# Kernel optimization log

Measured on AMD Instinct MI355X. Metric: run time of the kernel, lower is better.

The kernel has to match this reference:

```python
import jax, jax.numpy as jnp
import numpy as np

B, H, L, P = 16, 256, 8192, 64  # batch, d_input, seq_len, d_state


def setup_inputs() -> dict:
    key = jax.random.key(0)
    k1, k2, k3, k4, k5, k6 = jax.random.split(key, 6)
    u = jax.random.normal(k1, (B, H, L), dtype=jnp.float32)
    # diagonal SSM poles on an annulus inside the unit disk (stable discrete dynamics)
    radius = jax.random.uniform(k2, (P,), minval=0.5, maxval=0.99)
    theta = jax.random.uniform(k3, (P,), minval=0.0, maxval=2.0 * np.pi)
    A_re = (radius * jnp.cos(theta)).astype(jnp.float32)
    A_im = (radius * jnp.sin(theta)).astype(jnp.float32)
    # combined input/output mixing W = C*B, complex (H, P)
    BC_re = (jax.random.normal(k4, (H, P)) / np.sqrt(P)).astype(jnp.float32)
    BC_im = (jax.random.normal(k5, (H, P)) / np.sqrt(P)).astype(jnp.float32)
    # D skip vector: uniform_ring(min_radius=0.0, max_radius=1.0, field='real')
    D = jax.random.uniform(k6, (H,), minval=0.0, maxval=1.0, dtype=jnp.float32)
    return {"u": u, "A_re": A_re, "A_im": A_im, "BC_re": BC_re, "BC_im": BC_im, "D": D}


def reference(u, A_re, A_im, BC_re, BC_im, D):
    # Vandermonde kernel: k[h, l] = sum_p BC[h, p] * A[p]**l, computed stably via exp(l*log A)
    A = jax.lax.complex(A_re, A_im)                      # (P,)
    logA = jnp.log(A)                                    # (P,) complex
    ell = jnp.arange(L, dtype=jnp.float32)               # (L,)
    V = jnp.exp(logA[:, None] * ell[None, :])            # (P, L) complex Vandermonde
    BC = jax.lax.complex(BC_re, BC_im)                   # (H, P)
    k = jnp.einsum('hp,pl->hl', BC, V)                   # (H, L) complex kernel
    # circular FFT convolution (same-length fft/ifft as the torch code)
    u_s = jnp.fft.fft(u, axis=-1)                        # (B, H, L) complex
    k_s = jnp.fft.fft(k, axis=-1)                        # (H, L) complex
    y = jnp.fft.ifft(u_s * k_s[None, :, :], axis=-1).real
    y = y + D[None, :, None] * u                         # D*u skip
    return jnp.tanh(y)                                   # activation (dropout=0 -> identity)
```

## Files before the change

### kernel.cpp

```cpp
#include <hip/hip_runtime.h>
#include <cmath>


typedef _Float16 half8 __attribute__((ext_vector_type(8)));
typedef _Float16 half4v __attribute__((ext_vector_type(4)));
typedef _Float16 half2v __attribute__((ext_vector_type(2)));
typedef float floatx16 __attribute__((ext_vector_type(16)));

#define NC 64
#define CM 128
#define A2_BYTES ((size_t)256 * 128 * 256 * 2)
#define W_BYTES  ((size_t)128 * 128 * 2)
#define AM_OFF   (A2_BYTES + W_BYTES)

#define SWH(r, c) ((((r) << 7)) | ((c) ^ (((r) & 15) << 3)))

__device__ __forceinline__ float fast_tanh(float x) {
    float e2 = __expf(2.0f * x);
    return 1.0f - 2.0f / (e2 + 1.0f);
}

__global__ void fftconv_prep(const float* __restrict__ A_re, const float* __restrict__ A_im,
                             const float* __restrict__ BC_re, const float* __restrict__ BC_im,
                             const float* __restrict__ Dv, char* __restrict__ ws) {
    __shared__ float rr[64], th[64], br[64], bi[64];
    __shared__ float kk[CM];
    const int h = blockIdx.x, tid = threadIdx.x;
    if (tid < 64) {
        float x = A_re[tid], y = A_im[tid];
        rr[tid] = log2f(sqrtf(x * x + y * y));
        th[tid] = atan2f(y, x);
        br[tid] = BC_re[h * 64 + tid];
        bi[tid] = BC_im[h * 64 + tid];
    }
    __syncthreads();
    if (tid < CM) {
        float d = (float)tid, s = 0.f;
        for (int p = 0; p < 64; ++p) {
            float mag = exp2f(d * rr[p]);
            float ang = d * th[p];
            s += mag * (br[p] * cosf(ang) - bi[p] * sinf(ang));
        }
        kk[tid] = s;
    }
    __syncthreads();
    _Float16* A2 = (_Float16*)ws + (size_t)h * 128 * 256;
    const float Dh = Dv[h];
    for (int idx = tid; idx < 128 * 128; idx += 256) {
        int r = idx >> 7, pc = idx & 127, p = pc & 63;
        float e = (float)(r + 1);
        float mag = exp2f(e * rr[p]);
        float ang = e * th[p];
        float cr = mag * cosf(ang), ci = mag * sinf(ang);
        float val = (pc < 64) ? (br[p] * cr - bi[p] * ci) : -(br[p] * ci + bi[p] * cr);
        int cn = ((pc & 63) << 1) | (pc >> 6);
        A2[r * 256 + cn] = (_Float16)val;
    }
    for (int idx = tid; idx < 128 * 128; idx += 256) {
        int r = idx >> 7, j = idx & 127;
        float v = (j <= r) ? kk[r - j] : 0.f;
        if (j == r) v += Dh;
        A2[r * 256 + CM + j] = (_Float16)v;
    }
    if (h == 0) {
        _Float16* W = (_Float16*)(ws + A2_BYTES);
        for (int idx = tid; idx < 128 * 128; idx += 256) {
            int pc = idx >> 7, j = idx & 127, p = pc & 63;
            float e = (float)(127 - j);
            float mag = exp2f(e * rr[p]);
            float ang = e * th[p];
            float v = (pc < 64) ? mag * cosf(ang) : mag * sinf(ang);
            int rn = ((pc & 63) << 1) | (pc >> 6);
            W[rn * 128 + j] = (_Float16)v;
        }
        if (tid < 64) {
            float mag = exp2f(128.f * rr[tid]);
            float ang = 128.f * th[tid];
            float* aM = (float*)(ws + AM_OFF);
            aM[tid] = mag * cosf(ang);
            aM[64 + tid] = mag * sinf(ang);
        }
    }
}

__global__ __launch_bounds__(256, 3)
void fftconv_main(const float* __restrict__ u, const char* __restrict__ ws,
                  float* __restrict__ out) {
    __shared__ __align__(16) _Float16 u16[2][NC * CM];
    __shared__ __align__(16) _Float16 S16[NC * CM];

    const int tid = threadIdx.x;
    const int lane = tid & 63;
    const int wv = tid >> 6;
    const int h = blockIdx.x & 255;
    const int bbg = blockIdx.x >> 8;

    const int mrow = (wv << 5) + (lane & 31);
    const int kh = (lane >> 5) << 3;
    const int ncol = lane & 31;

    const _Float16* Wg = (const _Float16*)(ws + A2_BYTES) + (size_t)mrow * CM + kh;
    const _Float16* Ag = (const _Float16*)ws + ((size_t)h * CM + mrow) * 256 + kh;

    const float* ub0 = u + ((size_t)((bbg * 2 + 0) * 256) + h) * 8192;
    const float* ub1 = u + ((size_t)((bbg * 2 + 1) * 256) + h) * 8192;

    float4 uvA[8];
#pragma unroll
    for (int i = 0; i < 8; ++i) uvA[i] = ((const float4*)ub0)[i * 256 + tid];
    half8 wf[8], tf[8];
#pragma unroll
    for (int s = 0; s < 8; ++s) wf[s] = *(const half8*)(Wg + (s << 4));
#pragma unroll
    for (int s = 0; s < 8; ++s) tf[s] = *(const half8*)(Ag + CM + (s << 4));

#pragma unroll
    for (int i = 0; i < 8; ++i) {
        int e4 = i * 256 + tid;
        int c = e4 >> 5, j = (e4 << 2) & 127;
        half4v hv = { (_Float16)uvA[i].x, (_Float16)uvA[i].y,
                      (_Float16)uvA[i].z, (_Float16)uvA[i].w };
        *(half4v*)&u16[0][SWH(c, j)] = hv;
    }
    float4 uvB[8];
#pragma unroll
    for (int i = 0; i < 8; ++i) uvB[i] = ((const float4*)ub1)[i * 256 + tid];
    half8 gf[8];
    __syncthreads();

#pragma unroll
    for (int sq = 0; sq < 2; ++sq) {
        const _Float16* ub16 = u16[sq];

        {
            floatx16 a0 = {}; floatx16 a1 = {};
#pragma unroll
            for (int s = 0; s < 8; ++s) {
                int k0 = (s << 4) + kh;
                half8 b0 = *(const half8*)&ub16[SWH(ncol, k0)];
                half8 b1 = *(const half8*)&ub16[SWH(ncol + 32, k0)];
                a0 = __builtin_amdgcn_mfma_f32_32x32x16_f16(wf[s], b0, a0, 0, 0, 0);
                a1 = __builtin_amdgcn_mfma_f32_32x32x16_f16(wf[s], b1, a1, 0, 0, 0);
            }
            const int pc0 = (wv << 5) + ((lane >> 5) << 2);
#pragma unroll
            for (int g = 0; g < 4; ++g) {
                half4v h0 = { (_Float16)a0[4 * g + 0], (_Float16)a0[4 * g + 1],
                              (_Float16)a0[4 * g + 2], (_Float16)a0[4 * g + 3] };
                *(half4v*)&S16[SWH(ncol, pc0 + 8 * g)] = h0;
                half4v h1 = { (_Float16)a1[4 * g + 0], (_Float16)a1[4 * g + 1],
                              (_Float16)a1[4 * g + 2], (_Float16)a1[4 * g + 3] };
                *(half4v*)&S16[SWH(ncol + 32, pc0 + 8 * g)] = h1;
            }
        }
        if (sq == 0) {
#pragma unroll
            for (int i = 0; i < 8; ++i) {
                int e4 = i * 256 + tid;
                int c = e4 >> 5, j = (e4 << 2) & 127;
                half4v hv = { (_Float16)uvB[i].x, (_Float16)uvB[i].y,
                              (_Float16)uvB[i].z, (_Float16)uvB[i].w };
                *(half4v*)&u16[1][SWH(c, j)] = hv;
            }
        }
        __syncthreads();

        float er[16], ei[16];
        {
            const float* aM = (const float*)(ws + AM_OFF);
            const float amr = aM[lane], ami = aM[64 + lane];
            const int cbase = wv << 4;
            float sr = 0.f, si = 0.f, pr = 1.f, pi = 0.f;
#pragma unroll
            for (int d = 0; d < 8; ++d) {
                int cc = (cbase - 1 - d) & 63;
                half2v xv = *(const half2v*)&S16[SWH(cc, lane << 1)];
                float xr = (float)xv.x, xi = (float)xv.y;
                sr = fmaf(pr, xr, fmaf(-pi, xi, sr));
                si = fmaf(pr, xi, fmaf(pi, xr, si));
                float npr = pr * amr - pi * ami;
                float npi = pr * ami + pi * amr;
                pr = npr; pi = npi;
            }
            er[0] = sr; ei[0] = si;
#pragma unroll
            for (int i = 1; i < 16; ++i) {
                half2v xv = *(const half2v*)&S16[SWH(cbase + i - 1, lane << 1)];
                float xr = (float)xv.x, xi = (float)xv.y;
                er[i] = fmaf(amr, er[i - 1], fmaf(-ami, ei[i - 1], xr));
                ei[i] = fmaf(amr, ei[i - 1], fmaf(ami, er[i - 1], xi));
            }
        }
        __syncthreads();

        if (sq == 0) {
#pragma unroll
            for (int s = 0; s < 8; ++s) gf[s] = *(const half8*)(Ag + (s << 4));
        }

#pragma unroll
        for (int i = 0; i < 16; ++i) {
            int c = (wv << 4) + i;
            half2v ev = { (_Float16)er[i], (_Float16)ei[i] };
            *(half2v*)&S16[SWH(c, lane << 1)] = ev;
        }
        __syncthreads();

        {
            floatx16 y0 = {}; floatx16 y1 = {};
#pragma unroll
            for (int s = 0; s < 8; ++s) {
                int k0 = (s << 4) + kh;
                half8 b0 = *(const half8*)&S16[SWH(ncol, k0)];
                half8 b1 = *(const half8*)&S16[SWH(ncol + 32, k0)];
                y0 = __builtin_amdgcn_mfma_f32_32x32x16_f16(gf[s], b0, y0, 0, 0, 0);
                y1 = __builtin_amdgcn_mfma_f32_32x32x16_f16(gf[s], b1, y1, 0, 0, 0);
            }
#pragma unroll
            for (int s = 0; s < 8; ++s) {
                int k0 = (s << 4) + kh;
                half8 b0 = *(const half8*)&ub16[SWH(ncol, k0)];
                half8 b1 = *(const half8*)&ub16[SWH(ncol + 32, k0)];
                y0 = __builtin_amdgcn_mfma_f32_32x32x16_f16(tf[s], b0, y0, 0, 0, 0);
                y1 = __builtin_amdgcn_mfma_f32_32x32x16_f16(tf[s], b1, y1, 0, 0, 0);
            }
            float* yb = out + ((size_t)((bbg * 2 + sq) * 256) + h) * 8192;
            const int r0 = (wv << 5) + ((lane >> 5) << 2);
#pragma unroll
            for (int g = 0; g < 4; ++g) {
                float4 o0;
                o0.x = fast_tanh(y0[4 * g + 0]); o0.y = fast_tanh(y0[4 * g + 1]);
                o0.z = fast_tanh(y0[4 * g + 2]); o0.w = fast_tanh(y0[4 * g + 3]);
                *(float4*)(yb + (size_t)ncol * CM + r0 + 8 * g) = o0;
                float4 o1;
                o1.x = fast_tanh(y1[4 * g + 0]); o1.y = fast_tanh(y1[4 * g + 1]);
                o1.z = fast_tanh(y1[4 * g + 2]); o1.w = fast_tanh(y1[4 * g + 3]);
                *(float4*)(yb + (size_t)(ncol + 32) * CM + r0 + 8 * g) = o1;
            }
        }
        if (sq == 0) __syncthreads();
    }
}

extern "C" void kernel_launch(void* const* d_in, const int* in_sizes, int n_in,
                              void* d_out, int out_size, void* d_ws, size_t ws_size,
                              hipStream_t stream) {
    const float* u     = (const float*)d_in[0];
    const float* A_re  = (const float*)d_in[1];
    const float* A_im  = (const float*)d_in[2];
    const float* BC_re = (const float*)d_in[3];
    const float* BC_im = (const float*)d_in[4];
    const float* Dv    = (const float*)d_in[5];
    float* out = (float*)d_out;
    char* ws = (char*)d_ws;

    hipLaunchKernelGGL(fftconv_prep, dim3(256), dim3(256), 0, stream,
                       A_re, A_im, BC_re, BC_im, Dv, ws);
    hipLaunchKernelGGL(fftconv_main, dim3(2048), dim3(256), 0, stream,
                       u, ws, out);
}
```

Baseline: 350.9 us.

## Stream four sequences per block with async global-to-LDS DMA prefetch

Each block now handles four batch sequences instead of two, so the grid is halved and the per-(h) W/A fragments are loaded once and reused across more sequences. Input rows are fetched with global_load_lds directly into a swizzled fp32 LDS tile. The fetch for the next sequence is issued mid-iteration so it overlaps the scan and the second GEMM. The chunk scan is fused into one streaming loop without er/ei register arrays, and barriers use explicit lgkmcnt waits. This trades occupancy (launch bounds 3 to 2, larger LDS) and half the grid parallelism for fewer redundant loads and overlapped memory traffic.

Result: no change. 355.1 us (+1.2%).

```diff
diff --git a/kernel.cpp b/kernel.cpp
--- a/kernel.cpp
+++ b/kernel.cpp
@@ -9,15 +9,29 @@
 
 #define NC 64
 #define CM 128
+#define NSEQ 4
 #define A2_BYTES ((size_t)256 * 128 * 256 * 2)
 #define W_BYTES  ((size_t)128 * 128 * 2)
 #define AM_OFF   (A2_BYTES + W_BYTES)
 
 #define SWH(r, c) ((((r) << 7)) | ((c) ^ (((r) & 15) << 3)))
+#define SWF(c, q4) (((c) << 7) | ((((q4) ^ ((c) & 31))) << 2))
+
+#define BAR_LGKM() do { \
+    asm volatile("s_waitcnt lgkmcnt(0)" ::: "memory"); \
+    __builtin_amdgcn_sched_barrier(0); \
+    __builtin_amdgcn_s_barrier(); \
+} while (0)
 
 __device__ __forceinline__ float fast_tanh(float x) {
     float e2 = __expf(2.0f * x);
     return 1.0f - 2.0f / (e2 + 1.0f);
+}
+
+__device__ __forceinline__ void dma16(const void* g, void* l) {
+    __builtin_amdgcn_global_load_lds(
+        (const __attribute__((address_space(1))) void*)g,
+        (__attribute__((address_space(3))) void*)l, 16, 0, 0);
 }
 
 __global__ void fftconv_prep(const float* __restrict__ A_re, const float* __restrict__ A_im,
@@ -83,10 +97,11 @@
     }
 }
 
-__global__ __launch_bounds__(256, 3)
+__global__ __launch_bounds__(256, 2)
 void fftconv_main(const float* __restrict__ u, const char* __restrict__ ws,
                   float* __restrict__ out) {
-    __shared__ __align__(16) _Float16 u16[2][NC * CM];
+    __shared__ __align__(16) float    u32t[NC * CM];
+    __shared__ __align__(16) _Float16 u16t[NC * CM];
     __shared__ __align__(16) _Float16 S16[NC * CM];
 
     const int tid = threadIdx.x;
@@ -101,44 +116,48 @@
 
     const _Float16* Wg = (const _Float16*)(ws + A2_BYTES) + (size_t)mrow * CM + kh;
     const _Float16* Ag = (const _Float16*)ws + ((size_t)h * CM + mrow) * 256 + kh;
-
-    const float* ub0 = u + ((size_t)((bbg * 2 + 0) * 256) + h) * 8192;
-    const float* ub1 = u + ((size_t)((bbg * 2 + 1) * 256) + h) * 8192;
-
-    float4 uvA[8];
-#pragma unroll
-    for (int i = 0; i < 8; ++i) uvA[i] = ((const float4*)ub0)[i * 256 + tid];
-    half8 wf[8], tf[8];
+    const float* aM = (const float*)(ws + AM_OFF);
+    const float amr = aM[lane], ami = aM[64 + lane];
+
+    half8 wf[8], tf[8], gf[8];
 #pragma unroll
     for (int s = 0; s < 8; ++s) wf[s] = *(const half8*)(Wg + (s << 4));
 #pragma unroll
     for (int s = 0; s < 8; ++s) tf[s] = *(const half8*)(Ag + CM + (s << 4));
-
-#pragma unroll
-    for (int i = 0; i < 8; ++i) {
-        int e4 = i * 256 + tid;
-        int c = e4 >> 5, j = (e4 << 2) & 127;
-        half4v hv = { (_Float16)uvA[i].x, (_Float16)uvA[i].y,
-                      (_Float16)uvA[i].z, (_Float16)uvA[i].w };
-        *(half4v*)&u16[0][SWH(c, j)] = hv;
-    }
-    float4 uvB[8];
-#pragma unroll
-    for (int i = 0; i < 8; ++i) uvB[i] = ((const float4*)ub1)[i * 256 + tid];
-    half8 gf[8];
+#pragma unroll
+    for (int s = 0; s < 8; ++s) gf[s] = *(const half8*)(Ag + (s << 4));
+
+    {
+        const float* ub = u + ((size_t)((bbg * NSEQ + 0) * 256) + h) * 8192;
+#pragma unroll
+        for (int q = 0; q < 8; ++q) {
+            int c = (wv << 4) + (q << 1) + (lane >> 5);
+            int q4 = (lane & 31) ^ (c & 31);
+            dma16(ub + (c << 7) + (q4 << 2), u32t + (((wv << 4) + (q << 1)) << 7));
+        }
+    }
     __syncthreads();
 
-#pragma unroll
-    for (int sq = 0; sq < 2; ++sq) {
-        const _Float16* ub16 = u16[sq];
-
+#pragma unroll 1
+    for (int sq = 0; sq < NSEQ; ++sq) {
         {
             floatx16 a0 = {}; floatx16 a1 = {};
 #pragma unroll
             for (int s = 0; s < 8; ++s) {
                 int k0 = (s << 4) + kh;
-                half8 b0 = *(const half8*)&ub16[SWH(ncol, k0)];
-                half8 b1 = *(const half8*)&ub16[SWH(ncol + 32, k0)];
+                int q4 = k0 >> 2;
+                float4 xa = *(const float4*)&u32t[SWF(ncol, q4)];
+                float4 xb = *(const float4*)&u32t[SWF(ncol, q4 + 1)];
+                float4 ya = *(const float4*)&u32t[SWF(ncol + 32, q4)];
+                float4 yb2 = *(const float4*)&u32t[SWF(ncol + 32, q4 + 1)];
+                half8 b0 = { (_Float16)xa.x, (_Float16)xa.y, (_Float16)xa.z, (_Float16)xa.w,
+                             (_Float16)xb.x, (_Float16)xb.y, (_Float16)xb.z, (_Float16)xb.w };
+                half8 b1 = { (_Float16)ya.x, (_Float16)ya.y, (_Float16)ya.z, (_Float16)ya.w,
+                             (_Float16)yb2.x, (_Float16)yb2.y, (_Float16)yb2.z, (_Float16)yb2.w };
+                if ((s >> 1) == wv) {
+                    *(half8*)&u16t[SWH(ncol, k0)] = b0;
+                    *(half8*)&u16t[SWH(ncol + 32, k0)] = b1;
+                }
                 a0 = __builtin_amdgcn_mfma_f32_32x32x16_f16(wf[s], b0, a0, 0, 0, 0);
                 a1 = __builtin_amdgcn_mfma_f32_32x32x16_f16(wf[s], b1, a1, 0, 0, 0);
             }
@@ -153,58 +172,44 @@
                 *(half4v*)&S16[SWH(ncol + 32, pc0 + 8 * g)] = h1;
             }
         }
-        if (sq == 0) {
-#pragma unroll
-            for (int i = 0; i < 8; ++i) {
-                int e4 = i * 256 + tid;
-                int c = e4 >> 5, j = (e4 << 2) & 127;
-                half4v hv = { (_Float16)uvB[i].x, (_Float16)uvB[i].y,
-                              (_Float16)uvB[i].z, (_Float16)uvB[i].w };
-                *(half4v*)&u16[1][SWH(c, j)] = hv;
-            }
-        }
-        __syncthreads();
-
-        float er[16], ei[16];
-        {
-            const float* aM = (const float*)(ws + AM_OFF);
-            const float amr = aM[lane], ami = aM[64 + lane];
-            const int cbase = wv << 4;
-            float sr = 0.f, si = 0.f, pr = 1.f, pi = 0.f;
-#pragma unroll
-            for (int d = 0; d < 8; ++d) {
-                int cc = (cbase - 1 - d) & 63;
-                half2v xv = *(const half2v*)&S16[SWH(cc, lane << 1)];
-                float xr = (float)xv.x, xi = (float)xv.y;
-                sr = fmaf(pr, xr, fmaf(-pi, xi, sr));
-                si = fmaf(pr, xi, fmaf(pi, xr, si));
-                float npr = pr * amr - pi * ami;
-                float npi = pr * ami + pi * amr;
-                pr = npr; pi = npi;
-            }
-            er[0] = sr; ei[0] = si;
-#pragma unroll
-            for (int i = 1; i < 16; ++i) {
-                half2v xv = *(const half2v*)&S16[SWH(cbase + i - 1, lane << 1)];
-                float xr = (float)xv.x, xi = (float)xv.y;
-                er[i] = fmaf(amr, er[i - 1], fmaf(-ami, ei[i - 1], xr));
-                ei[i] = fmaf(amr, ei[i - 1], fmaf(ami, er[i - 1], xi));
-            }
-        }
-        __syncthreads();
-
-        if (sq == 0) {
-#pragma unroll
-            for (int s = 0; s < 8; ++s) gf[s] = *(const half8*)(Ag + (s << 4));
-        }
-
+        BAR_LGKM();
+
+        if (sq + 1 < NSEQ) {
+            const float* ub = u + ((size_t)((bbg * NSEQ + sq + 1) * 256) + h) * 8192;
+#pragma unroll
+            for (int q = 0; q < 8; ++q) {
+                int c = (wv << 4) + (q << 1) + (lane >> 5);
+                int q4 = (lane & 31) ^ (c & 31);
+                dma16(ub + (c << 7) + (q4 << 2), u32t + (((wv << 4) + (q << 1)) << 7));
+            }
+        }
+
+        const int cbase = wv << 4;
+        float sr = 0.f, si = 0.f, pr = 1.f, pi = 0.f;
+#pragma unroll
+        for (int d = 0; d < 8; ++d) {
+            int cc = (cbase - 1 - d) & 63;
+            half2v xv = *(const half2v*)&S16[SWH(cc, lane << 1)];
+            float xr = (float)xv.x, xi = (float)xv.y;
+            sr = fmaf(pr, xr, fmaf(-pi, xi, sr));
+            si = fmaf(pr, xi, fmaf(pi, xr, si));
+            float npr = pr * amr - pi * ami;
+            float npi = pr * ami + pi * amr;
+            pr = npr; pi = npi;
+        }
+        BAR_LGKM();
 #pragma unroll
         for (int i = 0; i < 16; ++i) {
-            int c = (wv << 4) + i;
-            half2v ev = { (_Float16)er[i], (_Float16)ei[i] };
+            int c = cbase + i;
+            half2v xv = *(const half2v*)&S16[SWH(c, lane << 1)];
+            half2v ev = { (_Float16)sr, (_Float16)si };
             *(half2v*)&S16[SWH(c, lane << 1)] = ev;
-        }
-        __syncthreads();
+            float xr = (float)xv.x, xi = (float)xv.y;
+            float nr = fmaf(amr, sr, fmaf(-ami, si, xr));
+            float ni = fmaf(amr, si, fmaf(ami, sr, xi));
+            sr = nr; si = ni;
+        }
+        BAR_LGKM();
 
         {
             floatx16 y0 = {}; floatx16 y1 = {};
@@ -219,12 +224,12 @@
 #pragma unroll
             for (int s = 0; s < 8; ++s) {
                 int k0 = (s << 4) + kh;
-                half8 b0 = *(const half8*)&ub16[SWH(ncol, k0)];
-                half8 b1 = *(const half8*)&ub16[SWH(ncol + 32, k0)];
+                half8 b0 = *(const half8*)&u16t[SWH(ncol, k0)];
+                half8 b1 = *(const half8*)&u16t[SWH(ncol + 32, k0)];
                 y0 = __builtin_amdgcn_mfma_f32_32x32x16_f16(tf[s], b0, y0, 0, 0, 0);
                 y1 = __builtin_amdgcn_mfma_f32_32x32x16_f16(tf[s], b1, y1, 0, 0, 0);
             }
-            float* yb = out + ((size_t)((bbg * 2 + sq) * 256) + h) * 8192;
+            float* yb = out + ((size_t)((bbg * NSEQ + sq) * 256) + h) * 8192;
             const int r0 = (wv << 5) + ((lane >> 5) << 2);
 #pragma unroll
             for (int g = 0; g < 4; ++g) {
@@ -238,7 +243,7 @@
                 *(float4*)(yb + (size_t)(ncol + 32) * CM + r0 + 8 * g) = o1;
             }
         }
-        if (sq == 0) __syncthreads();
+        __syncthreads();
     }
 }
 
@@ -256,6 +261,6 @@
 
     hipLaunchKernelGGL(fftconv_prep, dim3(256), dim3(256), 0, stream,
                        A_re, A_im, BC_re, BC_im, Dv, ws);
-    hipLaunchKernelGGL(fftconv_main, dim3(2048), dim3(256), 0, stream,
+    hipLaunchKernelGGL(fftconv_main, dim3(1024), dim3(256), 0, stream,
                        u, ws, out);
 }
```
